# Kernel optimization log

Hardware: AMD Instinct MI355X
Metric: run time of the kernel (lower is better)

Reference implementation:

```python
import jax, jax.numpy as jnp
import numpy as np

EMBED_DIM = 768
NUM_HEADS = 12
HEAD_DIM = EMBED_DIM // NUM_HEADS


def setup_inputs() -> dict:
    key = jax.random.key(0)
    k_x, k_wqkv, k_bqkv, k_wp, k_bp = jax.random.split(key, 5)
    B, S, D = 4, 2048, EMBED_DIM
    # nn.Linear default init scale ~ 1/sqrt(fan_in); exact distribution irrelevant for a reference
    lim = 1.0 / np.sqrt(D)
    x = jax.random.normal(k_x, (B, S, D), dtype=jnp.float32)
    w_qkv = jax.random.uniform(k_wqkv, (D, 3 * D), jnp.float32, -lim, lim)
    b_qkv = jax.random.uniform(k_bqkv, (3 * D,), jnp.float32, -lim, lim)
    w_proj = jax.random.uniform(k_wp, (D, D), jnp.float32, -lim, lim)
    b_proj = jax.random.uniform(k_bp, (D,), jnp.float32, -lim, lim)
    return {"x": x, "w_qkv": w_qkv, "b_qkv": b_qkv, "w_proj": w_proj, "b_proj": b_proj}


def reference(x, w_qkv, b_qkv, w_proj, b_proj):
    B, S, D = x.shape
    H, Hd = NUM_HEADS, HEAD_DIM
    qkv = x @ w_qkv + b_qkv                      # [B,S,3D]
    qkv = qkv.reshape(B, S, 3, H, Hd)
    qkv = jnp.transpose(qkv, (2, 0, 3, 1, 4))     # [3,B,H,S,Hd]
    q, k, v = qkv[0], qkv[1], qkv[2]
    scale = 1.0 / np.sqrt(Hd).astype(np.float32)
    scores = jnp.einsum("bhsd,bhtd->bhst", q, k) * scale  # [B,H,S,S]
    attn = jax.nn.softmax(scores, axis=-1)
    out = jnp.einsum("bhst,bhtd->bhsd", attn, v)  # [B,H,S,Hd]
    out = jnp.transpose(out, (0, 2, 1, 3)).reshape(B, S, D)
    return out @ w_proj + b_proj
```

## Files before the change

### kernel.cpp

```cpp
#include <hip/hip_runtime.h>


typedef _Float16 f16;
typedef _Float16 f16x8 __attribute__((ext_vector_type(8)));
typedef _Float16 f16x4 __attribute__((ext_vector_type(4)));
typedef float f32x4 __attribute__((ext_vector_type(4)));

#define BQ 4
#define SQ 2048
#define DQ 768
#define HQ 12
#define HD 64
#define M_TOK (BQ*SQ)
#define KVB 64
#define QSCALE 0.18033688f
#define THR_LOG2 11.5f

__device__ __forceinline__ void gld_lds16(const f16* g, f16* l) {
  __builtin_amdgcn_global_load_lds((const __attribute__((address_space(1))) void*)g,
                                   (__attribute__((address_space(3))) void*)l,
                                   16, 0, 0);
}

__global__ void cvt_x(const float* __restrict__ x, f16* __restrict__ xh, int n) {
  int i = (blockIdx.x * blockDim.x + threadIdx.x) * 4;
  if (i < n) {
    float4 v = *(const float4*)(x + i);
    f16x4 o = { (f16)v.x, (f16)v.y, (f16)v.z, (f16)v.w };
    *(f16x4*)(xh + i) = o;
  }
}

__global__ void cvt_transpose(const float* __restrict__ w, f16* __restrict__ wt, int K, int N) {
  __shared__ float tile[32][33];
  int nb = blockIdx.x * 32, kb = blockIdx.y * 32;
  int tx = threadIdx.x & 31, ty = threadIdx.x >> 5;
  for (int r = ty; r < 32; r += 8)
    tile[r][tx] = w[(size_t)(kb + r) * N + nb + tx];
  __syncthreads();
  for (int r = ty; r < 32; r += 8)
    wt[(size_t)(nb + r) * K + kb + tx] = (f16)tile[tx][r];
}

template<int MODE>
__global__ __launch_bounds__(256, 2)
void gemm128(const f16* __restrict__ A, const f16* __restrict__ Bt,
             const float* __restrict__ bias, float* __restrict__ Cf,
             f16* __restrict__ Qb, f16* __restrict__ Kb, f16* __restrict__ Vt,
             int M, int N, int K, int nbx)
{
  __shared__ f16 Ash[128 * 32];
  __shared__ f16 Bsh[128 * 32];
  const int tid = threadIdx.x;
  const int bid = blockIdx.x;
  const int nb = bid % nbx, mb = bid / nbx;
  const int m0 = mb * 128, n0 = nb * 128;
  const int lane = tid & 63, wid = tid >> 6;
  const int wr = wid >> 1, wc = wid & 1;
  const int l16 = lane & 15, l4 = lane >> 4;

  f32x4 acc[4][4] = {};

  const int f0 = tid, f1 = tid + 256;
  const f16* a0 = A + (size_t)(m0 + (f0 >> 2)) * K + (f0 & 3) * 8;
  const f16* a1 = A + (size_t)(m0 + (f1 >> 2)) * K + (f1 & 3) * 8;
  const f16* b0 = Bt + (size_t)(n0 + (f0 >> 2)) * K + (f0 & 3) * 8;
  const f16* b1 = Bt + (size_t)(n0 + (f1 >> 2)) * K + (f1 & 3) * 8;
  f16* lA0 = Ash + f0 * 8; f16* lA1 = Ash + f1 * 8;
  f16* lB0 = Bsh + f0 * 8; f16* lB1 = Bsh + f1 * 8;

  for (int k0 = 0; k0 < K; k0 += 32) {
    gld_lds16(a0 + k0, lA0);
    gld_lds16(a1 + k0, lA1);
    gld_lds16(b0 + k0, lB0);
    gld_lds16(b1 + k0, lB1);
    __syncthreads();
    f16x8 af[4], bfr[4];
    #pragma unroll
    for (int m = 0; m < 4; ++m)
      af[m] = *(const f16x8*)(Ash + (wr * 64 + m * 16 + l16) * 32 + l4 * 8);
    #pragma unroll
    for (int n = 0; n < 4; ++n)
      bfr[n] = *(const f16x8*)(Bsh + (wc * 64 + n * 16 + l16) * 32 + l4 * 8);
    #pragma unroll
    for (int m = 0; m < 4; ++m)
      #pragma unroll
      for (int n = 0; n < 4; ++n)
        acc[m][n] = __builtin_amdgcn_mfma_f32_16x16x32_f16(af[m], bfr[n], acc[m][n], 0, 0, 0);
    __syncthreads();
  }

  const int cbase = n0 + wc * 64;
  const int rbase = m0 + wr * 64;
  if (MODE == 1) {
    #pragma unroll
    for (int n = 0; n < 4; ++n) {
      int c = cbase + n * 16 + l16;
      float bv = bias[c];
      #pragma unroll
      for (int m = 0; m < 4; ++m)
        #pragma unroll
        for (int r = 0; r < 4; ++r) {
          int rr = rbase + m * 16 + l4 * 4 + r;
          Cf[(size_t)rr * N + c] = acc[m][n][r] + bv;
        }
    }
  } else {
    #pragma unroll
    for (int n = 0; n < 4; ++n) {
      int c = cbase + n * 16 + l16;
      float bv = bias[c];
      int which = c / DQ;
      int rem = c - which * DQ;
      int h = rem >> 6, hd = rem & 63;
      #pragma unroll
      for (int m = 0; m < 4; ++m) {
        int rr0 = rbase + m * 16 + l4 * 4;
        int b = rr0 >> 11, s = rr0 & 2047;
        size_t bh = (size_t)(b * HQ + h);
        if (which == 2) {
          f16x4 ov = { (f16)(acc[m][n][0] + bv), (f16)(acc[m][n][1] + bv),
                       (f16)(acc[m][n][2] + bv), (f16)(acc[m][n][3] + bv) };
          *(f16x4*)(Vt + (bh * HD + hd) * SQ + s) = ov;
        } else if (which == 0) {
          #pragma unroll
          for (int r = 0; r < 4; ++r)
            Qb[(bh * SQ + s + r) * HD + hd] = (f16)((acc[m][n][r] + bv) * QSCALE);
        } else {
          #pragma unroll
          for (int r = 0; r < 4; ++r)
            Kb[(bh * SQ + s + r) * HD + hd] = (f16)(acc[m][n][r] + bv);
        }
      }
    }
  }
}

__device__ __forceinline__ int permK(int p) {
  return ((p & 16) << 1) | (((p >> 2) & 3) << 3) | ((p & 32) >> 3) | (p & 3);
}

__global__ __launch_bounds__(256, 3)
void attn(const f16* __restrict__ Qb, const f16* __restrict__ Kb,
          const f16* __restrict__ Vt, f16* __restrict__ O)
{
  __shared__ f16 Ksh[2][KVB * HD];
  __shared__ f16 Vsh[2][HD * KVB];
  const int tid = threadIdx.x, lane = tid & 63, wid = tid >> 6;
  const int l16 = lane & 15, l4 = lane >> 4;

  const int nwg = gridDim.x;
  const int cpx = nwg >> 3;
  const int swz = (blockIdx.x & 7) * cpx + (blockIdx.x >> 3);
  const int qt = swz & 15, bh = swz >> 4;
  const int b = bh / HQ, h = bh - b * HQ;
  const f16* q  = Qb + (size_t)bh * SQ * HD;
  const f16* kp = Kb + (size_t)bh * SQ * HD;
  const f16* vp = Vt + (size_t)bh * HD * SQ;
  const int s0 = qt * 128 + wid * 32;

  f16x8 qf[2][2];
  #pragma unroll
  for (int g = 0; g < 2; ++g)
    #pragma unroll
    for (int kk = 0; kk < 2; ++kk)
      qf[g][kk] = *(const f16x8*)(q + (size_t)(s0 + g * 16 + l16) * HD + kk * 32 + l4 * 8);

  f32x4 oacc[2][4] = {};
  float mrun[2] = { -1e30f, -1e30f }, lrun[2] = { 0.f, 0.f };

  const int p0 = tid >> 3, p1 = (tid >> 3) + 32;
  const int scS = ((tid & 7) ^ (p0 & 7)) * 8;
  const int kr0 = permK(p0), kr1 = permK(p1);

#define STAGE(buf, t0)                                                        \
  do {                                                                        \
    gld_lds16(kp + (size_t)((t0) + kr0) * HD + scS, Ksh[buf] + tid * 8);      \
    gld_lds16(kp + (size_t)((t0) + kr1) * HD + scS, Ksh[buf] + (tid + 256) * 8);\
    gld_lds16(vp + (size_t)p0 * SQ + (t0) + scS,   Vsh[buf] + tid * 8);       \
    gld_lds16(vp + (size_t)p1 * SQ + (t0) + scS,   Vsh[buf] + (tid + 256) * 8);\
  } while (0)

#define COMPUTE(buf)                                                          \
  do {                                                                        \
    f32x4 sacc[2][4] = {};                                                    \
    __builtin_amdgcn_s_setprio(1);                                            \
    _Pragma("unroll")                                                         \
    for (int kk = 0; kk < 2; ++kk) {                                          \
      f16x8 kf[4];                                                            \
      _Pragma("unroll")                                                       \
      for (int n = 0; n < 4; ++n)                                             \
        kf[n] = *(const f16x8*)(Ksh[buf] + (n * 16 + l16) * HD +              \
                                ((kk * 32 + l4 * 8) ^ ((l16 & 7) * 8)));      \
      _Pragma("unroll")                                                       \
      for (int n = 0; n < 4; ++n) {                                           \
        sacc[0][n] = __builtin_amdgcn_mfma_f32_16x16x32_f16(kf[n], qf[0][kk], sacc[0][n], 0, 0, 0); \
        sacc[1][n] = __builtin_amdgcn_mfma_f32_16x16x32_f16(kf[n], qf[1][kk], sacc[1][n], 0, 0, 0); \
      }                                                                       \
    }                                                                         \
    __builtin_amdgcn_s_setprio(0);                                            \
    f16x8 bfr[2][2];                                                          \
    _Pragma("unroll")                                                         \
    for (int g = 0; g < 2; ++g) {                                             \
      float rm = -1e30f;                                                      \
      _Pragma("unroll")                                                       \
      for (int n = 0; n < 4; ++n)                                             \
        rm = fmaxf(rm, fmaxf(fmaxf(sacc[g][n][0], sacc[g][n][1]),             \
                             fmaxf(sacc[g][n][2], sacc[g][n][3])));           \
      rm = fmaxf(rm, __shfl_xor(rm, 16));                                     \
      rm = fmaxf(rm, __shfl_xor(rm, 32));                                     \
      if (!__all(rm - mrun[g] <= THR_LOG2)) {                                 \
        float mn = fmaxf(mrun[g], rm);                                        \
        float corr = __builtin_amdgcn_exp2f(mrun[g] - mn);                    \
        lrun[g] *= corr;                                                      \
        _Pragma("unroll")                                                     \
        for (int n = 0; n < 4; ++n)                                           \
          oacc[g][n] *= corr;                                                 \
        mrun[g] = mn;                                                         \
      }                                                                       \
      float mref = mrun[g];                                                   \
      float ps = 0.f;                                                         \
      _Pragma("unroll")                                                       \
      for (int n = 0; n < 4; ++n)                                             \
        _Pragma("unroll")                                                     \
        for (int r = 0; r < 4; ++r) {                                         \
          float pv = __builtin_amdgcn_exp2f(sacc[g][n][r] - mref);            \
          bfr[g][n & 1][(n >> 1) * 4 + r] = (f16)pv;                          \
          ps += pv;                                                           \
        }                                                                     \
      ps += __shfl_xor(ps, 16);                                               \
      ps += __shfl_xor(ps, 32);                                               \
      lrun[g] += ps;                                                          \
    }                                                                         \
    __builtin_amdgcn_s_setprio(1);                                            \
    _Pragma("unroll")                                                         \
    for (int kk = 0; kk < 2; ++kk) {                                          \
      f16x8 vf[4];                                                            \
      _Pragma("unroll")                                                       \
      for (int n = 0; n < 4; ++n)                                             \
        vf[n] = *(const f16x8*)(Vsh[buf] + (n * 16 + l16) * KVB +             \
                                ((kk * 32 + l4 * 8) ^ ((l16 & 7) * 8)));      \
      _Pragma("unroll")                                                       \
      for (int n = 0; n < 4; ++n) {                                           \
        oacc[0][n] = __builtin_amdgcn_mfma_f32_16x16x32_f16(vf[n], bfr[0][kk], oacc[0][n], 0, 0, 0); \
        oacc[1][n] = __builtin_amdgcn_mfma_f32_16x16x32_f16(vf[n], bfr[1][kk], oacc[1][n], 0, 0, 0); \
      }                                                                       \
    }                                                                         \
    __builtin_amdgcn_s_setprio(0);                                            \
  } while (0)

  STAGE(0, 0);
  __syncthreads();
  for (int t0 = 0; t0 < SQ; t0 += 2 * KVB) {
    STAGE(1, t0 + KVB);
    COMPUTE(0);
    __syncthreads();
    if (t0 + 2 * KVB < SQ) STAGE(0, t0 + 2 * KVB);
    COMPUTE(1);
    __syncthreads();
  }
#undef STAGE
#undef COMPUTE

  #pragma unroll
  for (int g = 0; g < 2; ++g) {
    float inv = 1.f / lrun[g];
    const int s = s0 + g * 16 + l16;
    f16* obase = O + ((size_t)b * SQ + s) * DQ + h * HD + l4 * 4;
    #pragma unroll
    for (int n = 0; n < 4; ++n) {
      f16x4 ov = { (f16)(oacc[g][n][0] * inv), (f16)(oacc[g][n][1] * inv),
                   (f16)(oacc[g][n][2] * inv), (f16)(oacc[g][n][3] * inv) };
      *(f16x4*)(obase + n * 16) = ov;
    }
  }
}

extern "C" void kernel_launch(void* const* d_in, const int* in_sizes, int n_in,
                              void* d_out, int out_size, void* d_ws, size_t ws_size,
                              hipStream_t stream) {
  const float* x      = (const float*)d_in[0];
  const float* w_qkv  = (const float*)d_in[1];
  const float* b_qkv  = (const float*)d_in[2];
  const float* w_proj = (const float*)d_in[3];
  const float* b_proj = (const float*)d_in[4];
  float* out = (float*)d_out;

  char* ws = (char*)d_ws;
  f16* xh     = (f16*)ws; ws += (size_t)M_TOK * DQ * 2;
  f16* wqkvT  = (f16*)ws; ws += (size_t)3 * DQ * DQ * 2;
  f16* wprojT = (f16*)ws; ws += (size_t)DQ * DQ * 2;
  f16* Qb     = (f16*)ws; ws += (size_t)M_TOK * DQ * 2;
  f16* Kb     = (f16*)ws; ws += (size_t)M_TOK * DQ * 2;
  f16* Vt     = (f16*)ws; ws += (size_t)M_TOK * DQ * 2;
  f16* AO     = xh;

  cvt_x<<<(M_TOK * DQ) / (256 * 4), 256, 0, stream>>>(x, xh, M_TOK * DQ);
  cvt_transpose<<<dim3((3 * DQ) / 32, DQ / 32), 256, 0, stream>>>(w_qkv, wqkvT, DQ, 3 * DQ);
  cvt_transpose<<<dim3(DQ / 32, DQ / 32), 256, 0, stream>>>(w_proj, wprojT, DQ, DQ);

  gemm128<0><<<(M_TOK / 128) * (3 * DQ / 128), 256, 0, stream>>>(
      xh, wqkvT, b_qkv, nullptr, Qb, Kb, Vt, M_TOK, 3 * DQ, DQ, 3 * DQ / 128);

  attn<<<BQ * HQ * (SQ / 128), 256, 0, stream>>>(Qb, Kb, Vt, AO);

  gemm128<1><<<(M_TOK / 128) * (DQ / 128), 256, 0, stream>>>(
      AO, wprojT, b_proj, out, nullptr, nullptr, nullptr, M_TOK, DQ, DQ, DQ / 128);
}
```

Baseline: 168.6 us.

## Double-buffer GEMM LDS tiles and merge conversion kernels into one launch

The GEMM main loop now uses two LDS buffers for the A and B tiles. It issues the global-to-LDS loads for the next K-step before computing on the current one, and drops one barrier per iteration, so memory latency can overlap the MFMA work. The three preprocessing kernels (x conversion and two weight transposes) are folded into a single launch that dispatches on block index, removing two kernel launches. Doubling the LDS footprint to 32KB per block could affect occupancy. The overlap also depends on the barrier waiting for the outstanding LDS DMA loads.

```diff
diff --git a/kernel.cpp b/kernel.cpp
--- a/kernel.cpp
+++ b/kernel.cpp
@@ -22,19 +22,29 @@
                                    16, 0, 0);
 }
 
-__global__ void cvt_x(const float* __restrict__ x, f16* __restrict__ xh, int n) {
-  int i = (blockIdx.x * blockDim.x + threadIdx.x) * 4;
-  if (i < n) {
+__global__ __launch_bounds__(256)
+void prep(const float* __restrict__ x, f16* __restrict__ xh,
+          const float* __restrict__ w_qkv, f16* __restrict__ wqkvT,
+          const float* __restrict__ w_proj, f16* __restrict__ wprojT)
+{
+  __shared__ float tile[32][33];
+  const int bid = blockIdx.x, tid = threadIdx.x;
+  if (bid < 6144) {
+    int i = (bid * 256 + tid) * 4;
     float4 v = *(const float4*)(x + i);
     f16x4 o = { (f16)v.x, (f16)v.y, (f16)v.z, (f16)v.w };
     *(f16x4*)(xh + i) = o;
-  }
-}
-
-__global__ void cvt_transpose(const float* __restrict__ w, f16* __restrict__ wt, int K, int N) {
-  __shared__ float tile[32][33];
-  int nb = blockIdx.x * 32, kb = blockIdx.y * 32;
-  int tx = threadIdx.x & 31, ty = threadIdx.x >> 5;
+    return;
+  }
+  const float* w; f16* wt; int K, N, nb, kb;
+  if (bid < 7872) {
+    int b2 = bid - 6144; w = w_qkv; wt = wqkvT; K = DQ; N = 3 * DQ;
+    nb = (b2 % 72) * 32; kb = (b2 / 72) * 32;
+  } else {
+    int b3 = bid - 7872; w = w_proj; wt = wprojT; K = DQ; N = DQ;
+    nb = (b3 % 24) * 32; kb = (b3 / 24) * 32;
+  }
+  int tx = tid & 31, ty = tid >> 5;
   for (int r = ty; r < 32; r += 8)
     tile[r][tx] = w[(size_t)(kb + r) * N + nb + tx];
   __syncthreads();
@@ -49,8 +59,8 @@
              f16* __restrict__ Qb, f16* __restrict__ Kb, f16* __restrict__ Vt,
              int M, int N, int K, int nbx)
 {
-  __shared__ f16 Ash[128 * 32];
-  __shared__ f16 Bsh[128 * 32];
+  __shared__ f16 Ash[2][128 * 32];
+  __shared__ f16 Bsh[2][128 * 32];
   const int tid = threadIdx.x;
   const int bid = blockIdx.x;
   const int nb = bid % nbx, mb = bid / nbx;
@@ -66,22 +76,27 @@
   const f16* a1 = A + (size_t)(m0 + (f1 >> 2)) * K + (f1 & 3) * 8;
   const f16* b0 = Bt + (size_t)(n0 + (f0 >> 2)) * K + (f0 & 3) * 8;
   const f16* b1 = Bt + (size_t)(n0 + (f1 >> 2)) * K + (f1 & 3) * 8;
-  f16* lA0 = Ash + f0 * 8; f16* lA1 = Ash + f1 * 8;
-  f16* lB0 = Bsh + f0 * 8; f16* lB1 = Bsh + f1 * 8;
-
+
+#define GSTAGE(buf, k0)                                   \
+  do {                                                    \
+    gld_lds16(a0 + (k0), Ash[buf] + f0 * 8);              \
+    gld_lds16(a1 + (k0), Ash[buf] + f1 * 8);              \
+    gld_lds16(b0 + (k0), Bsh[buf] + f0 * 8);              \
+    gld_lds16(b1 + (k0), Bsh[buf] + f1 * 8);              \
+  } while (0)
+
+  GSTAGE(0, 0);
+  __syncthreads();
   for (int k0 = 0; k0 < K; k0 += 32) {
-    gld_lds16(a0 + k0, lA0);
-    gld_lds16(a1 + k0, lA1);
-    gld_lds16(b0 + k0, lB0);
-    gld_lds16(b1 + k0, lB1);
-    __syncthreads();
+    const int buf = (k0 >> 5) & 1;
+    if (k0 + 32 < K) GSTAGE(buf ^ 1, k0 + 32);
     f16x8 af[4], bfr[4];
     #pragma unroll
     for (int m = 0; m < 4; ++m)
-      af[m] = *(const f16x8*)(Ash + (wr * 64 + m * 16 + l16) * 32 + l4 * 8);
+      af[m] = *(const f16x8*)(Ash[buf] + (wr * 64 + m * 16 + l16) * 32 + l4 * 8);
     #pragma unroll
     for (int n = 0; n < 4; ++n)
-      bfr[n] = *(const f16x8*)(Bsh + (wc * 64 + n * 16 + l16) * 32 + l4 * 8);
+      bfr[n] = *(const f16x8*)(Bsh[buf] + (wc * 64 + n * 16 + l16) * 32 + l4 * 8);
     #pragma unroll
     for (int m = 0; m < 4; ++m)
       #pragma unroll
@@ -89,6 +104,7 @@
         acc[m][n] = __builtin_amdgcn_mfma_f32_16x16x32_f16(af[m], bfr[n], acc[m][n], 0, 0, 0);
     __syncthreads();
   }
+#undef GSTAGE
 
   const int cbase = n0 + wc * 64;
   const int rbase = m0 + wr * 64;
@@ -295,9 +311,7 @@
   f16* Vt     = (f16*)ws; ws += (size_t)M_TOK * DQ * 2;
   f16* AO     = xh;
 
-  cvt_x<<<(M_TOK * DQ) / (256 * 4), 256, 0, stream>>>(x, xh, M_TOK * DQ);
-  cvt_transpose<<<dim3((3 * DQ) / 32, DQ / 32), 256, 0, stream>>>(w_qkv, wqkvT, DQ, 3 * DQ);
-  cvt_transpose<<<dim3(DQ / 32, DQ / 32), 256, 0, stream>>>(w_proj, wprojT, DQ, DQ);
+  prep<<<8448, 256, 0, stream>>>(x, xh, w_qkv, wqkvT, w_proj, wprojT);
 
   gemm128<0><<<(M_TOK / 128) * (3 * DQ / 128), 256, 0, stream>>>(
       xh, wqkvT, b_qkv, nullptr, Qb, Kb, Vt, M_TOK, 3 * DQ, DQ, 3 * DQ / 128);
```

Result: faster. 164.6 us (-2.3%).
